# Performance work log

Measured on AMD Instinct MI355X. Metric: run time of the kernel, lower is better.

The kernel has to match this reference:

```python
import math
import jax, jax.numpy as jnp
import numpy as np

T, C, NE = 4096, 2048, 2048
LAYER_ID, NUM_LAYERS = 12, 24


def setup_inputs() -> dict:
    key = jax.random.key(0)
    ks = jax.random.split(key, 5)
    r01 = LAYER_ID / (NUM_LAYERS - 1)
    r1a0 = 1.0 - LAYER_ID / NUM_LAYERS
    idx = jnp.arange(C, dtype=jnp.float32)
    # parameter inits faithful to the haiku module
    time_decay = -5.0 + 8.0 * (idx / (C - 1)) ** (0.7 + 1.3 * r01)
    time_first = jnp.full((C,), math.log(0.3), jnp.float32) + (jnp.mod(idx + 1, 3) - 1.0) * 0.5
    ddd = (idx / C)[None, :]  # [1, C]
    time_mix_k = jnp.power(ddd, r1a0)
    time_mix_v = jnp.power(ddd, r1a0) + 0.3 * r01
    time_mix_r = jnp.power(ddd, r1a0 * 0.5)
    scale = 0.02  # ~ 1/sqrt(fan_in), keeps exp(k) stable
    x = jax.random.normal(ks[0], (T, NE), jnp.float32)
    Wk = jax.random.normal(ks[1], (NE, C), jnp.float32) * scale
    Wv = jax.random.normal(ks[2], (NE, C), jnp.float32) * scale
    Wr = jax.random.normal(ks[3], (NE, C), jnp.float32) * scale
    Wo = jax.random.normal(ks[4], (C, NE), jnp.float32) * scale
    return {"x": x, "time_first": time_first, "time_decay": time_decay,
            "time_mix_k": time_mix_k, "time_mix_v": time_mix_v, "time_mix_r": time_mix_r,
            "Wk": Wk, "Wv": Wv, "Wr": Wr, "Wo": Wo}


def wkv_conv(w, u, k, v):
    # w,u: [C]; k,v: [T,C].  Faithful conv-trick WKV from the source module.
    w = -jnp.exp(w)
    kT, vT = k.T, v.T                      # [C, T]
    ek = jnp.exp(kT)
    a = ek * vT
    Tlen = kT.shape[1]
    Cn = kT.shape[0]
    # depthwise conv kernel: exp(decay * relative position), last tap = exp(u)
    td = jnp.arange(-(Tlen - 2), 1, dtype=kT.dtype)[None, :] * jnp.exp(w)[:, None]  # [C, T-1]
    td = jnp.concatenate([td, u[:, None]], axis=1)                                   # [C, T]
    kernel = jnp.exp(td)[:, None]           # [C, 1, T]
    a3 = jnp.pad(a[None], ((0, 0), (0, 0), (Tlen - 1, 0)))   # [1, C, 2T-1]
    k3 = jnp.pad(ek[None], ((0, 0), (0, 0), (Tlen - 1, 0)))
    num = jax.lax.conv_general_dilated(a3, kernel, (1,), [(0, 0)], feature_group_count=Cn)
    den = jax.lax.conv_general_dilated(k3, kernel, (1,), [(0, 0)], feature_group_count=Cn)
    return (num / den)[0]                   # [C, T]


def reference(x, time_first, time_decay, time_mix_k, time_mix_v, time_mix_r, Wk, Wv, Wr, Wo):
    xx = jnp.pad(x, ((1, 0), (0, 0)))[:-1]          # time shift
    xk = x * time_mix_k + xx * (1.0 - time_mix_k)
    xv = x * time_mix_v + xx * (1.0 - time_mix_v)
    xr = x * time_mix_r + xx * (1.0 - time_mix_r)
    k = xk @ Wk                                     # [T, C]
    v = xv @ Wv
    r = xr @ Wr
    sr = jax.nn.sigmoid(r)
    wkv = wkv_conv(time_decay, time_first, k, v).T  # [T, C]
    return (sr * wkv) @ Wo                          # [T, n_embd]
```

## Files before the change

kernel.cpp:

```cpp
#include <hip/hip_runtime.h>
#include <hip/hip_bf16.h>
#include <cstdint>
#include <cstddef>

#define T_LEN   4096
#define C_DIM   2048
#define NE_DIM  2048
#define CHUNK   32
#define NCHUNK  (T_LEN / CHUNK)
#define C2      (C_DIM / 2)

typedef __bf16 bf16;
typedef __attribute__((ext_vector_type(8))) __bf16 bf16x8;
typedef __attribute__((ext_vector_type(4))) __bf16 bf16x4;
typedef __attribute__((ext_vector_type(2))) __bf16 bf16x2;
typedef __attribute__((ext_vector_type(4))) float  f32x4;

__device__ __forceinline__ void gld_lds16(bf16* lds_dst, const bf16* g_src) {
  __builtin_amdgcn_global_load_lds(
      (__attribute__((address_space(1))) void*)(g_src),
      (__attribute__((address_space(3))) void*)(lds_dst),
      16, 0, 0);
}

__global__ __launch_bounds__(256) void mix_kernel(
    const float* __restrict__ x,
    const float* __restrict__ tmk, const float* __restrict__ tmv,
    const float* __restrict__ tmr,
    bf16* __restrict__ xk, bf16* __restrict__ xv, bf16* __restrict__ xr)
{
  int gid = blockIdx.x * 256 + threadIdx.x;
  int row = gid / (NE_DIM / 4);
  int e4  = gid % (NE_DIM / 4);
  const f32x4* x4 = (const f32x4*)x;
  f32x4 zero = {0.f, 0.f, 0.f, 0.f};
  f32x4 xc = x4[gid];
  f32x4 xp = (row > 0) ? x4[gid - NE_DIM / 4] : zero;
  f32x4 mk = ((const f32x4*)tmk)[e4];
  f32x4 mv = ((const f32x4*)tmv)[e4];
  f32x4 mr = ((const f32x4*)tmr)[e4];
  f32x4 vk = xc * mk + xp * (1.0f - mk);
  f32x4 vv = xc * mv + xp * (1.0f - mv);
  f32x4 vr = xc * mr + xp * (1.0f - mr);
  bf16x4 ok, ov, orr;
#pragma unroll
  for (int i = 0; i < 4; ++i) {
    ok[i]  = (bf16)vk[i];
    ov[i]  = (bf16)vv[i];
    orr[i] = (bf16)vr[i];
  }
  *(bf16x4*)(xk + (size_t)gid * 4) = ok;
  *(bf16x4*)(xv + (size_t)gid * 4) = ov;
  *(bf16x4*)(xr + (size_t)gid * 4) = orr;
}

__global__ __launch_bounds__(256) void wtrans(
    const float* __restrict__ W0, const float* __restrict__ W1,
    const float* __restrict__ W2, const float* __restrict__ W3,
    bf16* __restrict__ O0, bf16* __restrict__ O1,
    bf16* __restrict__ O2, bf16* __restrict__ O3)
{
  __shared__ float tile[32][33];
  int z = blockIdx.z;
  const float* W = (z == 0) ? W0 : (z == 1) ? W1 : (z == 2) ? W2 : W3;
  bf16* O        = (z == 0) ? O0 : (z == 1) ? O1 : (z == 2) ? O2 : O3;
  int bx = blockIdx.x * 32, by = blockIdx.y * 32;
  int tx = threadIdx.x, ty = threadIdx.y;
#pragma unroll
  for (int j = 0; j < 4; ++j)
    tile[ty + j * 8][tx] = W[(size_t)(by + ty + j * 8) * NE_DIM + bx + tx];
  __syncthreads();
#pragma unroll
  for (int j = 0; j < 4; ++j)
    O[(size_t)(bx + ty + j * 8) * NE_DIM + by + tx] = (bf16)tile[tx][ty + j * 8];
}

#define GK  2048
#define NT2 (GK / 64)

#define BARS() asm volatile("s_barrier" ::: "memory")
#define VMC(n) asm volatile("s_waitcnt vmcnt(" #n ")" ::: "memory")

#define STG(b, kt) do { \
  _Pragma("unroll") \
  for (int q = 0; q < 4; ++q) { \
    gld_lds16(&As[(b) * 8192 + q * 2048 + tid * 8], Ab + (size_t)(q * 32) * GK + (size_t)(kt) * 64); \
    gld_lds16(&Bs[(b) * 8192 + q * 2048 + tid * 8], Bb + (size_t)(q * 32) * GK + (size_t)(kt) * 64); \
  } \
} while (0)

#define COMPUTE(b) do { \
  bf16x8 af[4][2], bq[4][2]; \
  _Pragma("unroll") \
  for (int f = 0; f < 4; ++f) { \
    af[f][0] = *(const bf16x8*)&As[(b) * 8192 + aoff[f] + cx0]; \
    af[f][1] = *(const bf16x8*)&As[(b) * 8192 + aoff[f] + cx1]; \
    bq[f][0] = *(const bf16x8*)&Bs[(b) * 8192 + boff[f] + cx0]; \
    bq[f][1] = *(const bf16x8*)&Bs[(b) * 8192 + boff[f] + cx1]; \
  } \
  __builtin_amdgcn_s_setprio(1); \
  _Pragma("unroll") \
  for (int f = 0; f < 4; ++f) \
    _Pragma("unroll") \
    for (int g = 0; g < 4; ++g) { \
      acc[f][g] = __builtin_amdgcn_mfma_f32_16x16x32_bf16(af[f][0], bq[g][0], acc[f][g], 0, 0, 0); \
      acc[f][g] = __builtin_amdgcn_mfma_f32_16x16x32_bf16(af[f][1], bq[g][1], acc[f][g], 0, 0, 0); \
    } \
  __builtin_amdgcn_s_setprio(0); \
} while (0)

__global__ __launch_bounds__(256, 2) void gemm2(
    const bf16* __restrict__ A0p, const bf16* __restrict__ Bt0, float* __restrict__ C0p,
    const bf16* __restrict__ A1p, const bf16* __restrict__ Bt1, float* __restrict__ C1p,
    const bf16* __restrict__ A2p, const bf16* __restrict__ Bt2, float* __restrict__ C2p)
{
  __shared__ __align__(16) bf16 As[16384];
  __shared__ __align__(16) bf16 Bs[16384];
  const int z = blockIdx.y;
  const bf16* A  = (z == 0) ? A0p : (z == 1) ? A1p : A2p;
  const bf16* Bt = (z == 0) ? Bt0 : (z == 1) ? Bt1 : Bt2;
  float*      C  = (z == 0) ? C0p : (z == 1) ? C1p : C2p;

  const int tid  = threadIdx.x;
  const int lane = tid & 63, w = tid >> 6;
  const int wm = w >> 1, wn = w & 1;
  const int lr = lane & 15, kb = lane >> 4;

  int wg = blockIdx.x;
  int l  = (wg & 7) * 64 + (wg >> 3);
  int bm = l & 31, bn = l >> 5;

  const int sr = tid >> 3;
  const int sc = (tid & 7) ^ (sr & 7);
  const bf16* Ab = A  + ((size_t)(bm * 128) + sr) * GK + sc * 8;
  const bf16* Bb = Bt + ((size_t)(bn * 128) + sr) * GK + sc * 8;

  const int cx0 = (kb ^ (lr & 7)) * 8;
  const int cx1 = ((kb ^ (lr & 7)) ^ 4) * 8;
  int aoff[4], boff[4];
#pragma unroll
  for (int f = 0; f < 4; ++f) {
    aoff[f] = (wm * 64 + f * 16 + lr) * 64;
    boff[f] = (wn * 64 + f * 16 + lr) * 64;
  }

  f32x4 acc[4][4] = {};

  STG(0, 0);
  for (int t = 0; t < NT2 - 1; ++t) {
    const int cur = t & 1;
    STG(cur ^ 1, t + 1);
    VMC(8);
    BARS();
    COMPUTE(cur);
    BARS();
  }
  VMC(0);
  BARS();
  COMPUTE((NT2 - 1) & 1);

#pragma unroll
  for (int f = 0; f < 4; ++f)
#pragma unroll
    for (int g = 0; g < 4; ++g) {
      size_t r0 = (size_t)(bm * 128) + wm * 64 + f * 16 + kb * 4;
      int    c0 = bn * 128 + wn * 64 + g * 16 + lr;
#pragma unroll
      for (int j = 0; j < 4; ++j)
        C[(r0 + j) * C_DIM + c0] = acc[f][g][j];
    }
}

__global__ __launch_bounds__(256) void wkv_phase1(
    const float2* __restrict__ k2, const float2* __restrict__ v2,
    const float2* __restrict__ td2,
    float2* __restrict__ SA, float2* __restrict__ SB)
{
  int c = blockIdx.x * 256 + threadIdx.x;
  int m = blockIdx.y;
  float2 td = td2[c];
  float fx = __expf(-__expf(td.x)), fy = __expf(-__expf(td.y));
  float Dx = __expf(-fx), Dy = __expf(-fy);
  float sax = 0.f, say = 0.f, sbx = 0.f, sby = 0.f;
  size_t base = (size_t)m * CHUNK * C2 + c;
  for (int t = 0; t < CHUNK; ++t) {
    float2 kk = k2[base + (size_t)t * C2];
    float2 vv = v2[base + (size_t)t * C2];
    float ekx = __expf(kk.x), eky = __expf(kk.y);
    sax = Dx * sax + ekx * vv.x;  sbx = Dx * sbx + ekx;
    say = Dy * say + eky * vv.y;  sby = Dy * sby + eky;
  }
  SA[(size_t)m * C2 + c] = make_float2(sax, say);
  SB[(size_t)m * C2 + c] = make_float2(sbx, sby);
}

__global__ __launch_bounds__(256) void wkv_phase2(
    const float2* __restrict__ td2,
    const float2* __restrict__ SA, const float2* __restrict__ SB,
    float2* __restrict__ A0, float2* __restrict__ B0)
{
  int c = blockIdx.x * 256 + threadIdx.x;
  float2 td = td2[c];
  float fx = __expf(-__expf(td.x)), fy = __expf(-__expf(td.y));
  float DLx = __expf(-fx * (float)CHUNK), DLy = __expf(-fy * (float)CHUNK);
  float ax = 0.f, ay = 0.f, bx = 0.f, by = 0.f;
  for (int m = 0; m < NCHUNK; ++m) {
    A0[(size_t)m * C2 + c] = make_float2(ax, ay);
    B0[(size_t)m * C2 + c] = make_float2(bx, by);
    float2 sa = SA[(size_t)m * C2 + c];
    float2 sb = SB[(size_t)m * C2 + c];
    ax = DLx * ax + sa.x;  ay = DLy * ay + sa.y;
    bx = DLx * bx + sb.x;  by = DLy * by + sb.y;
  }
}

__global__ __launch_bounds__(256) void wkv_phase3(
    const float2* __restrict__ k2, const float2* __restrict__ v2,
    const float2* __restrict__ r2,
    const float2* __restrict__ td2, const float2* __restrict__ tf2,
    const float2* __restrict__ A0, const float2* __restrict__ B0,
    bf16* __restrict__ y)
{
  int c = blockIdx.x * 256 + threadIdx.x;
  int m = blockIdx.y;
  float2 td = td2[c], tf = tf2[c];
  float fx = __expf(-__expf(td.x)), fy = __expf(-__expf(td.y));
  float Dx = __expf(-fx), Dy = __expf(-fy);
  float eux = __expf(tf.x), euy = __expf(tf.y);
  float2 a0 = A0[(size_t)m * C2 + c], b0 = B0[(size_t)m * C2 + c];
  float ax = a0.x, ay = a0.y, bx = b0.x, by = b0.y;
  size_t base = (size_t)m * CHUNK * C2 + c;
  for (int t = 0; t < CHUNK; ++t) {
    size_t idx = base + (size_t)t * C2;
    float2 kk = k2[idx], vv = v2[idx], rr = r2[idx];
    float ekx = __expf(kk.x), eky = __expf(kk.y);
    float ex = eux * ekx,     ey = euy * eky;
    float wx = (ax + ex * vv.x) / (bx + ex);
    float wy = (ay + ey * vv.y) / (by + ey);
    float sx = 1.0f / (1.0f + __expf(-rr.x));
    float sy = 1.0f / (1.0f + __expf(-rr.y));
    bf16x2 o2; o2[0] = (bf16)(sx * wx); o2[1] = (bf16)(sy * wy);
    *(bf16x2*)&y[idx * 2] = o2;
    ax = Dx * ax + ekx * vv.x;  bx = Dx * bx + ekx;
    ay = Dy * ay + eky * vv.y;  by = Dy * by + eky;
  }
}

extern "C" void kernel_launch(void* const* d_in, const int* in_sizes, int n_in,
                              void* d_out, int out_size, void* d_ws, size_t ws_size,
                              hipStream_t stream)
{
  (void)in_sizes; (void)n_in; (void)out_size; (void)ws_size;
  const float* x   = (const float*)d_in[0];
  const float* tf  = (const float*)d_in[1];
  const float* td  = (const float*)d_in[2];
  const float* tmk = (const float*)d_in[3];
  const float* tmv = (const float*)d_in[4];
  const float* tmr = (const float*)d_in[5];
  const float* Wk  = (const float*)d_in[6];
  const float* Wv  = (const float*)d_in[7];
  const float* Wr  = (const float*)d_in[8];
  const float* Wo  = (const float*)d_in[9];
  float* out = (float*)d_out;

  char* ws = (char*)d_ws;
  size_t off = 0;
  auto alloc = [&](size_t bytes) {
    void* p = ws + off;
    off += (bytes + 255) & ~(size_t)255;
    return p;
  };
  const size_t TN  = (size_t)T_LEN * NE_DIM;
  const size_t WN  = (size_t)C_DIM * NE_DIM;

  bf16* xk   = (bf16*)alloc(TN * 2);
  bf16* xv   = (bf16*)alloc(TN * 2);
  bf16* xr   = (bf16*)alloc(TN * 2);
  bf16* WkT  = (bf16*)alloc(WN * 2);
  bf16* WvT  = (bf16*)alloc(WN * 2);
  bf16* WrT  = (bf16*)alloc(WN * 2);
  bf16* WoT  = (bf16*)alloc(WN * 2);
  float* kbuf = (float*)alloc(TN * 4);
  float* vbuf = (float*)alloc(TN * 4);
  float* rbuf = (float*)alloc(TN * 4);
  bf16*   y  = xk;
  float2* SA = (float2*)xv;
  float2* SB = SA + (size_t)NCHUNK * C2;
  float2* A0 = SB + (size_t)NCHUNK * C2;
  float2* B0 = A0 + (size_t)NCHUNK * C2;

  mix_kernel<<<dim3((unsigned)(TN / 4 / 256)), 256, 0, stream>>>(
      x, tmk, tmv, tmr, xk, xv, xr);
  wtrans<<<dim3(64, 64, 4), dim3(32, 8), 0, stream>>>(
      Wk, Wv, Wr, Wo, WkT, WvT, WrT, WoT);
  gemm2<<<dim3(512, 3), 256, 0, stream>>>(
      xk, WkT, kbuf, xv, WvT, vbuf, xr, WrT, rbuf);
  wkv_phase1<<<dim3(C2 / 256, NCHUNK), 256, 0, stream>>>(
      (const float2*)kbuf, (const float2*)vbuf, (const float2*)td, SA, SB);
  wkv_phase2<<<dim3(C2 / 256), 256, 0, stream>>>(
      (const float2*)td, SA, SB, A0, B0);
  wkv_phase3<<<dim3(C2 / 256, NCHUNK), 256, 0, stream>>>(
      (const float2*)kbuf, (const float2*)vbuf, (const float2*)rbuf,
      (const float2*)td, (const float2*)tf, A0, B0, y);
  gemm2<<<dim3(512, 1), 256, 0, stream>>>(
      y, WoT, out, y, WoT, out, y, WoT, out);
}
```

Measured before the change: 405.0 us.

## Triple-buffer GEMM with 32-wide K tiles and batch phase2 scan loads

The bf16 GEMM moves from double-buffered 64-wide K tiles to triple-buffered 32-wide K tiles. It uses a new XOR swizzle, less LDS per block, and launch bounds raised to 3 blocks per CU, so more loads stay in flight and occupancy rises. The phase2 chunk scan now loads 8 chunk states at once before the sequential recurrence, which hides global load latency. The trade-off is twice as many barriers per K step and fewer MFMAs between each sync.

Result: faster. 379.6 us (-6.3%).

```diff
diff --git a/kernel.cpp b/kernel.cpp
--- a/kernel.cpp
+++ b/kernel.cpp
@@ -76,46 +76,41 @@
 }
 
 #define GK  2048
-#define NT2 (GK / 64)
+#define NT3 (GK / 32)
 
 #define BARS() asm volatile("s_barrier" ::: "memory")
 #define VMC(n) asm volatile("s_waitcnt vmcnt(" #n ")" ::: "memory")
 
-#define STG(b, kt) do { \
-  _Pragma("unroll") \
-  for (int q = 0; q < 4; ++q) { \
-    gld_lds16(&As[(b) * 8192 + q * 2048 + tid * 8], Ab + (size_t)(q * 32) * GK + (size_t)(kt) * 64); \
-    gld_lds16(&Bs[(b) * 8192 + q * 2048 + tid * 8], Bb + (size_t)(q * 32) * GK + (size_t)(kt) * 64); \
-  } \
+#define STG(boff, kt) do { \
+  gld_lds16(&As[(boff) + tid * 8],        Ab + (size_t)(kt) * 32); \
+  gld_lds16(&As[(boff) + 2048 + tid * 8], Ab + (size_t)64 * GK + (size_t)(kt) * 32); \
+  gld_lds16(&Bs[(boff) + tid * 8],        Bb + (size_t)(kt) * 32); \
+  gld_lds16(&Bs[(boff) + 2048 + tid * 8], Bb + (size_t)64 * GK + (size_t)(kt) * 32); \
 } while (0)
 
-#define COMPUTE(b) do { \
-  bf16x8 af[4][2], bq[4][2]; \
+#define COMPUTE(boff) do { \
+  bf16x8 af[4], bq[4]; \
   _Pragma("unroll") \
   for (int f = 0; f < 4; ++f) { \
-    af[f][0] = *(const bf16x8*)&As[(b) * 8192 + aoff[f] + cx0]; \
-    af[f][1] = *(const bf16x8*)&As[(b) * 8192 + aoff[f] + cx1]; \
-    bq[f][0] = *(const bf16x8*)&Bs[(b) * 8192 + boff[f] + cx0]; \
-    bq[f][1] = *(const bf16x8*)&Bs[(b) * 8192 + boff[f] + cx1]; \
+    af[f] = *(const bf16x8*)&As[(boff) + aoff[f]]; \
+    bq[f] = *(const bf16x8*)&Bs[(boff) + bqo[f]]; \
   } \
   __builtin_amdgcn_s_setprio(1); \
   _Pragma("unroll") \
   for (int f = 0; f < 4; ++f) \
     _Pragma("unroll") \
-    for (int g = 0; g < 4; ++g) { \
-      acc[f][g] = __builtin_amdgcn_mfma_f32_16x16x32_bf16(af[f][0], bq[g][0], acc[f][g], 0, 0, 0); \
-      acc[f][g] = __builtin_amdgcn_mfma_f32_16x16x32_bf16(af[f][1], bq[g][1], acc[f][g], 0, 0, 0); \
-    } \
+    for (int g = 0; g < 4; ++g) \
+      acc[f][g] = __builtin_amdgcn_mfma_f32_16x16x32_bf16(af[f], bq[g], acc[f][g], 0, 0, 0); \
   __builtin_amdgcn_s_setprio(0); \
 } while (0)
 
-__global__ __launch_bounds__(256, 2) void gemm2(
+__global__ __launch_bounds__(256, 3) void gemm3(
     const bf16* __restrict__ A0p, const bf16* __restrict__ Bt0, float* __restrict__ C0p,
     const bf16* __restrict__ A1p, const bf16* __restrict__ Bt1, float* __restrict__ C1p,
     const bf16* __restrict__ A2p, const bf16* __restrict__ Bt2, float* __restrict__ C2p)
 {
-  __shared__ __align__(16) bf16 As[16384];
-  __shared__ __align__(16) bf16 Bs[16384];
+  __shared__ __align__(16) bf16 As[12288];
+  __shared__ __align__(16) bf16 Bs[12288];
   const int z = blockIdx.y;
   const bf16* A  = (z == 0) ? A0p : (z == 1) ? A1p : A2p;
   const bf16* Bt = (z == 0) ? Bt0 : (z == 1) ? Bt1 : Bt2;
@@ -130,34 +125,33 @@
   int l  = (wg & 7) * 64 + (wg >> 3);
   int bm = l & 31, bn = l >> 5;
 
-  const int sr = tid >> 3;
-  const int sc = (tid & 7) ^ (sr & 7);
-  const bf16* Ab = A  + ((size_t)(bm * 128) + sr) * GK + sc * 8;
-  const bf16* Bb = Bt + ((size_t)(bn * 128) + sr) * GK + sc * 8;
-
-  const int cx0 = (kb ^ (lr & 7)) * 8;
-  const int cx1 = ((kb ^ (lr & 7)) ^ 4) * 8;
-  int aoff[4], boff[4];
+  const int srow = tid >> 2;
+  const int gc   = (tid & 3) ^ ((tid >> 3) & 3);
+  const bf16* Ab = A  + ((size_t)(bm * 128) + srow) * GK + gc * 8;
+  const bf16* Bb = Bt + ((size_t)(bn * 128) + srow) * GK + gc * 8;
+
+  const int cxp = (kb ^ ((lr >> 1) & 3)) * 8;
+  int aoff[4], bqo[4];
 #pragma unroll
   for (int f = 0; f < 4; ++f) {
-    aoff[f] = (wm * 64 + f * 16 + lr) * 64;
-    boff[f] = (wn * 64 + f * 16 + lr) * 64;
+    aoff[f] = (wm * 64 + f * 16 + lr) * 32 + cxp;
+    bqo[f]  = (wn * 64 + f * 16 + lr) * 32 + cxp;
   }
 
   f32x4 acc[4][4] = {};
 
-  STG(0, 0);
-  for (int t = 0; t < NT2 - 1; ++t) {
-    const int cur = t & 1;
-    STG(cur ^ 1, t + 1);
+  STG(0, 0); STG(4096, 1);
+  int b0 = 0, b1 = 4096, b2 = 8192;
+  for (int t = 0; t < NT3 - 2; ++t) {
+    STG(b2, t + 2);
     VMC(8);
     BARS();
-    COMPUTE(cur);
+    COMPUTE(b0);
     BARS();
-  }
-  VMC(0);
-  BARS();
-  COMPUTE((NT2 - 1) & 1);
+    int tmp = b0; b0 = b1; b1 = b2; b2 = tmp;
+  }
+  VMC(4); BARS(); COMPUTE(b0); BARS();
+  VMC(0); BARS(); COMPUTE(b1);
 
 #pragma unroll
   for (int f = 0; f < 4; ++f)
@@ -204,13 +198,20 @@
   float fx = __expf(-__expf(td.x)), fy = __expf(-__expf(td.y));
   float DLx = __expf(-fx * (float)CHUNK), DLy = __expf(-fy * (float)CHUNK);
   float ax = 0.f, ay = 0.f, bx = 0.f, by = 0.f;
-  for (int m = 0; m < NCHUNK; ++m) {
-    A0[(size_t)m * C2 + c] = make_float2(ax, ay);
-    B0[(size_t)m * C2 + c] = make_float2(bx, by);
-    float2 sa = SA[(size_t)m * C2 + c];
-    float2 sb = SB[(size_t)m * C2 + c];
-    ax = DLx * ax + sa.x;  ay = DLy * ay + sa.y;
-    bx = DLx * bx + sb.x;  by = DLy * by + sb.y;
+  for (int m0 = 0; m0 < NCHUNK; m0 += 8) {
+    float2 sa[8], sb[8];
+#pragma unroll
+    for (int j = 0; j < 8; ++j) {
+      sa[j] = SA[(size_t)(m0 + j) * C2 + c];
+      sb[j] = SB[(size_t)(m0 + j) * C2 + c];
+    }
+#pragma unroll
+    for (int j = 0; j < 8; ++j) {
+      A0[(size_t)(m0 + j) * C2 + c] = make_float2(ax, ay);
+      B0[(size_t)(m0 + j) * C2 + c] = make_float2(bx, by);
+      ax = DLx * ax + sa[j].x;  ay = DLy * ay + sa[j].y;
+      bx = DLx * bx + sb[j].x;  by = DLy * by + sb[j].y;
+    }
   }
 }
 
@@ -293,7 +294,7 @@
       x, tmk, tmv, tmr, xk, xv, xr);
   wtrans<<<dim3(64, 64, 4), dim3(32, 8), 0, stream>>>(
       Wk, Wv, Wr, Wo, WkT, WvT, WrT, WoT);
-  gemm2<<<dim3(512, 3), 256, 0, stream>>>(
+  gemm3<<<dim3(512, 3), 256, 0, stream>>>(
       xk, WkT, kbuf, xv, WvT, vbuf, xr, WrT, rbuf);
   wkv_phase1<<<dim3(C2 / 256, NCHUNK), 256, 0, stream>>>(
       (const float2*)kbuf, (const float2*)vbuf, (const float2*)td, SA, SB);
@@ -302,6 +303,6 @@
   wkv_phase3<<<dim3(C2 / 256, NCHUNK), 256, 0, stream>>>(
       (const float2*)kbuf, (const float2*)vbuf, (const float2*)rbuf,
       (const float2*)td, (const float2*)tf, A0, B0, y);
-  gemm2<<<dim3(512, 1), 256, 0, stream>>>(
+  gemm3<<<dim3(512, 1), 256, 0, stream>>>(
       y, WoT, out, y, WoT, out, y, WoT, out);
 }
```
